# Kernel tuning notes

Hardware: AMD Instinct MI355X
Metric: run time of the kernel (lower is better)

The kernel has to match this reference:

```python
import jax, jax.numpy as jnp
import numpy as np

N, E, F_IN, F_E = 50000, 800000, 128, 16
R, H, C = 4, 4, 32            # num_relations, heads, out_channels
HC = H * C                     # 128
NEG_SLOPE = 0.2                # PyG RGATConv default negative_slope
EPS = 1e-16                    # PyG softmax epsilon


def rgat_conv(x, src, dst, edge_type, edge_attr, w, q, k, e, le, b, concat):
    """Faithful PyG RGATConv (additive-self-attention, across-relation, dim=1, aggr=add).
    x: [N,F]; w: [R,F,H*C]; q,k,e: [H*C,H]; le: [F_e,H*C]; b: bias."""
    n = x.shape[0]
    xw = jnp.einsum('nf,rfo->rno', x, w)              # [R,N,H*C] per-relation projections
    x_i = xw[edge_type, dst]                          # [E,H*C] target-node proj per edge
    x_j = xw[edge_type, src]                          # [E,H*C] source-node proj per edge
    qi = x_i @ q                                      # [E,H]
    kj = x_j @ k + (edge_attr @ le) @ e               # [E,H] (edge features folded into keys)
    alpha = jax.nn.leaky_relu(qi + kj, NEG_SLOPE)     # [E,H]
    # softmax over incoming edges of each destination node (across relations)
    amax = jax.ops.segment_max(alpha, dst, num_segments=n)
    ex = jnp.exp(alpha - amax[dst])
    denom = jax.ops.segment_sum(ex, dst, num_segments=n)
    alpha = ex / (denom[dst] + EPS)
    msg = alpha[:, :, None] * x_j.reshape(-1, H, C)   # [E,H,C]
    out = jax.ops.segment_sum(msg, dst, num_segments=n)  # [N,H,C] sum aggregation
    out = out.reshape(n, H * C) if concat else out.mean(axis=1)
    return out + b


def setup_inputs() -> dict:
    key = jax.random.key(0)
    ks = jax.random.split(key, 18)
    p = 0.05
    inp = {
        'x': jax.random.normal(ks[0], (N, F_IN), dtype=jnp.float32),
        'edge_index': jax.random.randint(ks[1], (2, E), 0, N, dtype=jnp.int64)
            if jax.config.jax_enable_x64 else jax.random.randint(ks[1], (2, E), 0, N).astype(jnp.int32),
        'edge_attr': jax.random.normal(ks[2], (E, F_E), dtype=jnp.float32),
        'edge_type': jax.random.randint(ks[3], (E,), 0, R).astype(jnp.int32),
        # conv1 params (in=F_IN, concat=True -> bias of size H*C)
        'w1': jax.random.normal(ks[4], (R, F_IN, HC), dtype=jnp.float32) * p,
        'q1': jax.random.normal(ks[5], (HC, H), dtype=jnp.float32) * p,
        'k1': jax.random.normal(ks[6], (HC, H), dtype=jnp.float32) * p,
        'e1': jax.random.normal(ks[7], (HC, H), dtype=jnp.float32) * p,
        'le1': jax.random.normal(ks[8], (F_E, HC), dtype=jnp.float32) * p,
        'b1': jnp.zeros((HC,), dtype=jnp.float32),
        # conv3 params (in=H*C=128, concat=False -> bias of size C)
        'w3': jax.random.normal(ks[9], (R, HC, HC), dtype=jnp.float32) * p,
        'q3': jax.random.normal(ks[10], (HC, H), dtype=jnp.float32) * p,
        'k3': jax.random.normal(ks[11], (HC, H), dtype=jnp.float32) * p,
        'e3': jax.random.normal(ks[12], (HC, H), dtype=jnp.float32) * p,
        'le3': jax.random.normal(ks[13], (F_E, HC), dtype=jnp.float32) * p,
        'b3': jnp.zeros((C,), dtype=jnp.float32),
    }
    return inp


def reference(x, edge_index, edge_attr, edge_type,
              w1, q1, k1, e1, le1, b1,
              w3, q3, k3, e3, le3, b3):
    src, dst = edge_index[0], edge_index[1]
    h = jax.nn.relu(rgat_conv(x, src, dst, edge_type, edge_attr,
                              w1, q1, k1, e1, le1, b1, concat=True))
    out = rgat_conv(h, src, dst, edge_type, edge_attr,
                    w3, q3, k3, e3, le3, b3, concat=False)
    return out
```

## Files before the change

kernel.cpp:

```cpp
#include <hip/hip_runtime.h>


#define NEG_SLOPE 0.2f
#define SOFT_EPS 1e-16f

typedef __attribute__((ext_vector_type(8))) short bf16x8;
typedef __attribute__((ext_vector_type(4))) float f32x4;
typedef __attribute__((ext_vector_type(4))) unsigned short u16x4;
typedef __attribute__((ext_vector_type(4))) _Float16 half4;
typedef __attribute__((ext_vector_type(8))) _Float16 half8;

__device__ __forceinline__ void bf16split(float f, unsigned short& h, unsigned short& l) {
  unsigned u = __float_as_uint(f);
  unsigned r = u + 0x7FFFu + ((u >> 16) & 1u);
  h = (unsigned short)(r >> 16);
  float fh = __uint_as_float(((unsigned)h) << 16);
  float d = f - fh;
  unsigned u2 = __float_as_uint(d);
  unsigned r2 = u2 + 0x7FFFu + ((u2 >> 16) & 1u);
  l = (unsigned short)(r2 >> 16);
}


__device__ __forceinline__ void hist_body(int id, const int* __restrict__ dst,
                                          int* __restrict__ deg, int E) {
  int e = id * 256 + (int)threadIdx.x;
  if (e < E) atomicAdd(&deg[dst[e]], 1);
}

__device__ __forceinline__ void convx_body(int id, const float* __restrict__ in,
                                           unsigned short* __restrict__ hi,
                                           unsigned short* __restrict__ lo, int total8) {
  int i = id * 256 + (int)threadIdx.x;
  if (i >= total8) return;
  const float4* p = (const float4*)in + (size_t)i * 2;
  float4 a = p[0], b = p[1];
  float v[8] = {a.x, a.y, a.z, a.w, b.x, b.y, b.z, b.w};
  bf16x8 hv, lv;
#pragma unroll
  for (int j = 0; j < 8; ++j) {
    unsigned short h, l;
    bf16split(v[j], h, l);
    hv[j] = (short)h; lv[j] = (short)l;
  }
  *(bf16x8*)(hi + (size_t)i * 8) = hv;
  *(bf16x8*)(lo + (size_t)i * 8) = lv;
}

__device__ __forceinline__ void convw_body(int idx, const float* __restrict__ w1,
                                           const float* __restrict__ w3,
                                           unsigned short* __restrict__ wF1h,
                                           unsigned short* __restrict__ wF1l,
                                           unsigned short* __restrict__ wF3h,
                                           unsigned short* __restrict__ wF3l) {
  if (idx >= 131072) return;
  int L = idx >> 16;
  int rem = idx & 65535;
  int r = rem >> 14, rem2 = rem & 16383, f = rem2 >> 7, o = rem2 & 127;
  const float* w = L ? w3 : w1;
  unsigned short* dh = L ? wF3h : wF1h;
  unsigned short* dl = L ? wF3l : wF1l;
  float v = w[(r * 128 + f) * 128 + o];
  unsigned short h, l;
  bf16split(v, h, l);
  int ot = o >> 4, c = o & 15, kc = f >> 5, q = (f >> 3) & 3, j = f & 7;
  int di = r * 16384 + ((((ot * 4 + kc) * 4 + q) * 16 + c) * 8 + j);
  dh[di] = h;
  dl[di] = l;
}

__device__ __forceinline__ void wqk_body(int idx, const float* __restrict__ w1,
                                         const float* __restrict__ q1, const float* __restrict__ k1,
                                         const float* __restrict__ w3, const float* __restrict__ q3,
                                         const float* __restrict__ k3, float* __restrict__ wqk) {
  if (idx >= 8192) return;
  int L = idx >> 12, rem = idx & 4095;
  int r = rem >> 10, rem2 = rem & 1023, f = rem2 >> 3, j = rem2 & 7;
  const float* w = L ? w3 : w1;
  const float* qk = (j < 4) ? (L ? q3 : q1) : (L ? k3 : k1);
  int h = j & 3;
  const float* wrow = w + (r * 128 + f) * 128;
  float acc = 0.f;
  for (int o = 0; o < 128; ++o) acc += wrow[o] * qk[o * 4 + h];
  wqk[idx] = acc;
}

__device__ __forceinline__ void lee_body(const float* __restrict__ le1, const float* __restrict__ e1,
                                         const float* __restrict__ le3, const float* __restrict__ e3,
                                         float* __restrict__ lee) {
  int t = threadIdx.x;
  if (t >= 128) return;
  const float* le = (t < 64) ? le1 : le3;
  const float* ee = (t < 64) ? e1 : e3;
  int u = t & 63, f = u >> 2, h = u & 3;
  float acc = 0.f;
  for (int o = 0; o < 128; ++o) acc += le[f * 128 + o] * ee[o * 4 + h];
  lee[t] = acc;
}

__global__ __launch_bounds__(256) void pre_kernel(
    const int* __restrict__ dst, int* __restrict__ deg, int E,
    const float* __restrict__ x, unsigned short* __restrict__ xhi,
    unsigned short* __restrict__ xlo, int total8,
    const float* __restrict__ w1, const float* __restrict__ q1, const float* __restrict__ k1,
    const float* __restrict__ w3, const float* __restrict__ q3, const float* __restrict__ k3,
    float* __restrict__ wqk,
    const float* __restrict__ le1, const float* __restrict__ e1,
    const float* __restrict__ le3, const float* __restrict__ e3, float* __restrict__ lee,
    unsigned short* __restrict__ wF1h, unsigned short* __restrict__ wF1l,
    unsigned short* __restrict__ wF3h, unsigned short* __restrict__ wF3l,
    int nAB, int eb, int cxb) {
  int bid = blockIdx.x;
  if (bid < nAB) {
    int id = bid >> 1;
    if (bid & 1) {
      if (id < eb) hist_body(id, dst, deg, E);
    } else {
      if (id < cxb) convx_body(id, x, xhi, xlo, total8);
    }
  } else {
    int b2 = bid - nAB;
    if (b2 < 512) {
      convw_body(b2 * 256 + (int)threadIdx.x, w1, w3, wF1h, wF1l, wF3h, wF3l);
    } else if (b2 < 544) {
      wqk_body((b2 - 512) * 256 + (int)threadIdx.x, w1, q1, k1, w3, q3, k3, wqk);
    } else {
      lee_body(le1, e1, le3, e3, lee);
    }
  }
}


__global__ __launch_bounds__(256) void scanA_kernel(const int* __restrict__ deg,
                                                    int* __restrict__ bsum, int N) {
  int b = blockIdx.x, t = threadIdx.x;
  int base = b * 1024 + t * 4;
  int s = 0;
#pragma unroll
  for (int j = 0; j < 4; ++j) {
    int i = base + j;
    if (i < N) s += deg[i];
  }
#pragma unroll
  for (int o = 1; o < 64; o <<= 1) s += __shfl_xor(s, o);
  __shared__ int wsum[4];
  if ((t & 63) == 0) wsum[t >> 6] = s;
  __syncthreads();
  if (t == 0) bsum[b] = wsum[0] + wsum[1] + wsum[2] + wsum[3];
}

__global__ __launch_bounds__(256) void scanB_kernel(const int* __restrict__ bsum,
                                                    int* __restrict__ boff,
                                                    int* __restrict__ row_start,
                                                    int nb, int N) {
  int t = threadIdx.x;
  int v = (t < nb) ? bsum[t] : 0;
  int inc = v;
#pragma unroll
  for (int o = 1; o < 64; o <<= 1) {
    int u = __shfl_up(inc, o);
    if ((t & 63) >= o) inc += u;
  }
  __shared__ int wt[4];
  if ((t & 63) == 63) wt[t >> 6] = inc;
  __syncthreads();
  int add = 0;
  for (int wv = 0; wv < (t >> 6); ++wv) add += wt[wv];
  inc += add;
  if (t < nb) boff[t] = inc - v;
  if (t == 255) row_start[N] = inc;
}

__global__ __launch_bounds__(256) void scanC_kernel(const int* __restrict__ deg,
                                                    const int* __restrict__ boff,
                                                    int* __restrict__ row_start,
                                                    int* __restrict__ cursor, int N) {
  int b = blockIdx.x, t = threadIdx.x;
  int base = b * 1024 + t * 4;
  int d[4];
  int s = 0;
#pragma unroll
  for (int j = 0; j < 4; ++j) {
    int i = base + j;
    d[j] = (i < N) ? deg[i] : 0;
    s += d[j];
  }
  int inc = s;
#pragma unroll
  for (int o = 1; o < 64; o <<= 1) {
    int u = __shfl_up(inc, o);
    if ((t & 63) >= o) inc += u;
  }
  __shared__ int wt[4];
  if ((t & 63) == 63) wt[t >> 6] = inc;
  __syncthreads();
  int add = boff[b];
  for (int wv = 0; wv < (t >> 6); ++wv) add += wt[wv];
  int off = add + inc - s;
#pragma unroll
  for (int j = 0; j < 4; ++j) {
    int i = base + j;
    if (i < N) {
      row_start[i] = off;
      cursor[i] = off;
      off += d[j];
    }
  }
}


__device__ __forceinline__ void scatter_body(int id, const int* __restrict__ src,
                                             const int* __restrict__ dst,
                                             const int* __restrict__ et,
                                             int* __restrict__ cursor,
                                             int4* __restrict__ es, int E) {
  int e = id * 256 + (int)threadIdx.x;
  if (e >= E) return;
  int d = dst[e];
  int pos = atomicAdd(&cursor[d], 1);
  es[pos] = make_int4(src[e], d, et[e], e);
}

__device__ __forceinline__ void qkx_body(int nbid, char* smem, const float* __restrict__ xin,
                                         const float* __restrict__ wqk, float* __restrict__ qn,
                                         float* __restrict__ kn, int N) {
  float* swqk = (float*)smem;
  int t = threadIdx.x;
#pragma unroll
  for (int j = 0; j < 16; ++j) {
    int i = j * 256 + t;
    swqk[(i >> 10) * 1032 + (i & 1023)] = wqk[i];
  }
  __syncthreads();
  int nb = nbid * 64;
  int rl = t >> 2, r = t & 3;
  int n = nb + rl;
  int nc = n < N ? n : N - 1;
  const float4* xr = (const float4*)(xin + (size_t)nc * 128);
  const float* wb = swqk + r * 1032;
  float aq0 = 0, aq1 = 0, aq2 = 0, aq3 = 0;
  float ak0 = 0, ak1 = 0, ak2 = 0, ak3 = 0;
#pragma unroll 4
  for (int f4 = 0; f4 < 32; ++f4) {
    float4 xv = xr[f4];
    const float* w0 = wb + f4 * 32;
    float4 qa = *(const float4*)(w0);
    float4 ka = *(const float4*)(w0 + 4);
    float4 qb = *(const float4*)(w0 + 8);
    float4 kb = *(const float4*)(w0 + 12);
    float4 qc = *(const float4*)(w0 + 16);
    float4 kc = *(const float4*)(w0 + 20);
    float4 qd = *(const float4*)(w0 + 24);
    float4 kd = *(const float4*)(w0 + 28);
    aq0 += xv.x * qa.x + xv.y * qb.x + xv.z * qc.x + xv.w * qd.x;
    aq1 += xv.x * qa.y + xv.y * qb.y + xv.z * qc.y + xv.w * qd.y;
    aq2 += xv.x * qa.z + xv.y * qb.z + xv.z * qc.z + xv.w * qd.z;
    aq3 += xv.x * qa.w + xv.y * qb.w + xv.z * qc.w + xv.w * qd.w;
    ak0 += xv.x * ka.x + xv.y * kb.x + xv.z * kc.x + xv.w * kd.x;
    ak1 += xv.x * ka.y + xv.y * kb.y + xv.z * kc.y + xv.w * kd.y;
    ak2 += xv.x * ka.z + xv.y * kb.z + xv.z * kc.z + xv.w * kd.z;
    ak3 += xv.x * ka.w + xv.y * kb.w + xv.z * kc.w + xv.w * kd.w;
  }
  if (n < N) {
    *(float4*)(qn + ((size_t)r * N + n) * 4) = make_float4(aq0, aq1, aq2, aq3);
    *(float4*)(kn + ((size_t)r * N + n) * 4) = make_float4(ak0, ak1, ak2, ak3);
  }
}

__global__ __launch_bounds__(256) void sc_kernel(
    const int* __restrict__ src, const int* __restrict__ dst, const int* __restrict__ et,
    int* __restrict__ cursor, int4* __restrict__ es, int E,
    const float* __restrict__ xin, const float* __restrict__ wqk,
    float* __restrict__ qn, float* __restrict__ kn, int N, int qxb) {
  extern __shared__ char smem[];
  int bid = blockIdx.x;
  int g = bid / 5, r5 = bid - g * 5;
  if (r5 == 4) {
    if (g < qxb) qkx_body(g, smem, xin, wqk, qn, kn, N);
  } else {
    scatter_body(g * 4 + r5, src, dst, et, cursor, es, E);
  }
}


__device__ __forceinline__ void ek2_body(int id, char* smem, const int4* __restrict__ es,
                                         const float* __restrict__ ea,
                                         const float* __restrict__ lee,
                                         float* __restrict__ eks1, float* __restrict__ eks3,
                                         int E) {
  float* sl = (float*)smem;
  if (threadIdx.x < 128) sl[threadIdx.x] = lee[threadIdx.x];
  __syncthreads();
  int i = id * 256 + (int)threadIdx.x;
  if (i >= E) return;
  int eid = es[i].w;
  const float4* a4 = (const float4*)(ea + (size_t)eid * 16);
  float a1[4] = {0, 0, 0, 0}, a3[4] = {0, 0, 0, 0};
#pragma unroll
  for (int ii = 0; ii < 4; ++ii) {
    float4 v = a4[ii];
    int f = ii * 4;
#pragma unroll
    for (int h = 0; h < 4; ++h) {
      a1[h] += v.x * sl[f * 4 + h] + v.y * sl[(f + 1) * 4 + h] +
               v.z * sl[(f + 2) * 4 + h] + v.w * sl[(f + 3) * 4 + h];
      a3[h] += v.x * sl[64 + f * 4 + h] + v.y * sl[64 + (f + 1) * 4 + h] +
               v.z * sl[64 + (f + 2) * 4 + h] + v.w * sl[64 + (f + 3) * 4 + h];
    }
  }
  *(float4*)(eks1 + (size_t)i * 4) = make_float4(a1[0], a1[1], a1[2], a1[3]);
  *(float4*)(eks3 + (size_t)i * 4) = make_float4(a3[0], a3[1], a3[2], a3[3]);
}

__device__ __forceinline__ void proj_body(int pid, char* smem,
                                          const unsigned short* __restrict__ xhi,
                                          const unsigned short* __restrict__ xlo,
                                          const unsigned short* __restrict__ wFh,
                                          const unsigned short* __restrict__ wFl,
                                          _Float16* __restrict__ xwh, int N) {
  bf16x8* wl_h = (bf16x8*)smem;
  bf16x8* wl_l = wl_h + 1024;
  int r = pid & 3;
  int h0 = (pid >> 2) & 1;
  int nb = (pid >> 3) * 128;
  int t = threadIdx.x;
  const bf16x8* srcH = (const bf16x8*)(wFh + r * 16384) + h0 * 1024;
  const bf16x8* srcL = (const bf16x8*)(wFl + r * 16384) + h0 * 1024;
#pragma unroll
  for (int j = 0; j < 4; ++j) {
    int i = j * 256 + t;
    wl_h[i] = srcH[i];
    wl_l[i] = srcL[i];
  }
  __syncthreads();

  int wv = t >> 6;
  int lane = t & 63;
  int c = lane & 15, q = lane >> 4;
  int nodebase = nb + wv * 32;
  int n0 = nodebase + c;
  int n1 = nodebase + 16 + c;
  int n0c = n0 < N ? n0 : N - 1;
  int n1c = n1 < N ? n1 : N - 1;

  f32x4 acc[4][2];
#pragma unroll
  for (int ot = 0; ot < 4; ++ot)
#pragma unroll
    for (int nt = 0; nt < 2; ++nt) acc[ot][nt] = (f32x4){0.f, 0.f, 0.f, 0.f};

  bf16x8 xb[2][4];
  {
    int k0 = q * 8;
    xb[0][0] = *(const bf16x8*)(xhi + (size_t)n0c * 128 + k0);
    xb[0][1] = *(const bf16x8*)(xlo + (size_t)n0c * 128 + k0);
    xb[0][2] = *(const bf16x8*)(xhi + (size_t)n1c * 128 + k0);
    xb[0][3] = *(const bf16x8*)(xlo + (size_t)n1c * 128 + k0);
  }
#pragma unroll
  for (int kc = 0; kc < 4; ++kc) {
    if (kc < 3) {
      int k0 = (kc + 1) * 32 + q * 8;
      xb[(kc + 1) & 1][0] = *(const bf16x8*)(xhi + (size_t)n0c * 128 + k0);
      xb[(kc + 1) & 1][1] = *(const bf16x8*)(xlo + (size_t)n0c * 128 + k0);
      xb[(kc + 1) & 1][2] = *(const bf16x8*)(xhi + (size_t)n1c * 128 + k0);
      xb[(kc + 1) & 1][3] = *(const bf16x8*)(xlo + (size_t)n1c * 128 + k0);
    }
    bf16x8 b0h = xb[kc & 1][0], b0l = xb[kc & 1][1];
    bf16x8 b1h = xb[kc & 1][2], b1l = xb[kc & 1][3];
#pragma unroll
    for (int ot = 0; ot < 4; ++ot) {
      int fi = ((ot * 4 + kc) * 4 + q) * 16 + c;
      bf16x8 ah = wl_h[fi];
      bf16x8 al = wl_l[fi];
      acc[ot][0] = __builtin_amdgcn_mfma_f32_16x16x32_bf16(ah, b0h, acc[ot][0], 0, 0, 0);
      acc[ot][0] = __builtin_amdgcn_mfma_f32_16x16x32_bf16(ah, b0l, acc[ot][0], 0, 0, 0);
      acc[ot][0] = __builtin_amdgcn_mfma_f32_16x16x32_bf16(al, b0h, acc[ot][0], 0, 0, 0);
      acc[ot][1] = __builtin_amdgcn_mfma_f32_16x16x32_bf16(ah, b1h, acc[ot][1], 0, 0, 0);
      acc[ot][1] = __builtin_amdgcn_mfma_f32_16x16x32_bf16(ah, b1l, acc[ot][1], 0, 0, 0);
      acc[ot][1] = __builtin_amdgcn_mfma_f32_16x16x32_bf16(al, b1h, acc[ot][1], 0, 0, 0);
    }
  }

#pragma unroll
  for (int nt = 0; nt < 2; ++nt) {
    int n = nodebase + nt * 16 + c;
    if (n < N) {
      _Float16* basep = xwh + ((size_t)r * N + n) * 128 + h0 * 64 + q * 4;
#pragma unroll
      for (int ot = 0; ot < 4; ++ot) {
        f32x4 a = acc[ot][nt];
        half4 hv;
        hv[0] = (_Float16)a.x; hv[1] = (_Float16)a.y;
        hv[2] = (_Float16)a.z; hv[3] = (_Float16)a.w;
        *(half4*)(basep + ot * 16) = hv;
      }
    }
  }
}

__global__ __launch_bounds__(256) void ep1_kernel(
    const int4* __restrict__ es, const float* __restrict__ ea, const float* __restrict__ lee,
    float* __restrict__ eks1, float* __restrict__ eks3, int E,
    const unsigned short* __restrict__ xhi, const unsigned short* __restrict__ xlo,
    const unsigned short* __restrict__ wFh, const unsigned short* __restrict__ wFl,
    _Float16* __restrict__ xwh, int N, int eb, int pjb) {
  extern __shared__ char smem[];
  int bid = blockIdx.x;
  int g = bid / 3, r3 = bid - g * 3;
  if (r3 == 0) {
    if (g < eb) ek2_body(g, smem, es, ea, lee, eks1, eks3, E);
  } else {
    int id = g * 2 + (r3 - 1);
    if (id < pjb) proj_body(id, smem, xhi, xlo, wFh, wFl, xwh, N);
  }
}

__global__ __launch_bounds__(256) void p2_kernel(
    const unsigned short* __restrict__ xhi, const unsigned short* __restrict__ xlo,
    const unsigned short* __restrict__ wFh, const unsigned short* __restrict__ wFl,
    _Float16* __restrict__ xwh, int N,
    const float* __restrict__ xin, const float* __restrict__ wqk,
    float* __restrict__ qn, float* __restrict__ kn, int pjb, int qxb) {
  extern __shared__ char smem[];
  int bid = blockIdx.x;
  int g = bid / 5, r5 = bid - g * 5;
  if (r5 == 4) {
    if (g < qxb) qkx_body(g, smem, xin, wqk, qn, kn, N);
  } else {
    int id = g * 4 + r5;
    if (id < pjb) proj_body(id, smem, xhi, xlo, wFh, wFl, xwh, N);
  }
}


__device__ __forceinline__ float4 edge_alpha(const int4* __restrict__ es,
                                             const float* __restrict__ qn,
                                             const float* __restrict__ kn,
                                             const float* __restrict__ eks,
                                             int i, int d, int N) {
  int4 v = es[i];
  float4 kv = *(const float4*)(kn + (v.z * N + v.x) * 4);
  float4 ev = ((const float4*)eks)[i];
  float4 q4 = *(const float4*)(qn + (v.z * N + d) * 4);
  float4 a = make_float4(q4.x + kv.x + ev.x, q4.y + kv.y + ev.y,
                         q4.z + kv.z + ev.z, q4.w + kv.w + ev.w);
  a.x = a.x > 0.f ? a.x : NEG_SLOPE * a.x;
  a.y = a.y > 0.f ? a.y : NEG_SLOPE * a.y;
  a.z = a.z > 0.f ? a.z : NEG_SLOPE * a.z;
  a.w = a.w > 0.f ? a.w : NEG_SLOPE * a.w;
  return a;
}

__device__ __forceinline__ float4 max4(float4 a, float4 b) {
  return make_float4(fmaxf(a.x, b.x), fmaxf(a.y, b.y), fmaxf(a.z, b.z), fmaxf(a.w, b.w));
}

__global__ __launch_bounds__(256) void agg_kernel(
    const int4* __restrict__ es, const int* __restrict__ row_start,
    const float* __restrict__ qn, const float* __restrict__ kn,
    const float* __restrict__ eks, float* __restrict__ alpha_s,
    const _Float16* __restrict__ xwh, const float* __restrict__ bias,
    float* __restrict__ out, unsigned short* __restrict__ xhi,
    unsigned short* __restrict__ xlo, int N, int concat) {
  int d = blockIdx.x * 16 + (threadIdx.x >> 4);
  if (d >= N) return;
  int ql = threadIdx.x & 15;
  int rs = row_start[d], re = row_start[d + 1];
  int deg = re - rs;
  int h = ql >> 2;

  float acc[8];
#pragma unroll
  for (int j = 0; j < 8; ++j) acc[j] = 0.f;
  float rden = 0.f;

  if (deg > 0) {
    float4 m = make_float4(-1e30f, -1e30f, -1e30f, -1e30f);
    float4 ar0 = m, ar1 = m, ar2 = m, ar3 = m;
    bool fast = (deg <= 64);
    bool v0 = ql < deg, v1 = 16 + ql < deg, v2 = 32 + ql < deg, v3 = 48 + ql < deg;
    if (fast) {
      int dm1 = deg - 1;
      int o0 = v0 ? ql : dm1;
      int o1 = v1 ? 16 + ql : dm1;
      int o2 = v2 ? 32 + ql : dm1;
      int o3 = v3 ? 48 + ql : dm1;
      float4 a0 = edge_alpha(es, qn, kn, eks, rs + o0, d, N);
      float4 a1 = edge_alpha(es, qn, kn, eks, rs + o1, d, N);
      float4 a2 = edge_alpha(es, qn, kn, eks, rs + o2, d, N);
      float4 a3 = edge_alpha(es, qn, kn, eks, rs + o3, d, N);
      if (v0) { ar0 = a0; m = max4(m, a0); }
      if (v1) { ar1 = a1; m = max4(m, a1); }
      if (v2) { ar2 = a2; m = max4(m, a2); }
      if (v3) { ar3 = a3; m = max4(m, a3); }
    } else {
      for (int i = rs + ql; i < re; i += 16) {
        float4 a = edge_alpha(es, qn, kn, eks, i, d, N);
        ((float4*)alpha_s)[i] = a;
        m = max4(m, a);
      }
    }
#pragma unroll
    for (int o = 1; o < 16; o <<= 1) {
      m.x = fmaxf(m.x, __shfl_xor(m.x, o));
      m.y = fmaxf(m.y, __shfl_xor(m.y, o));
      m.z = fmaxf(m.z, __shfl_xor(m.z, o));
      m.w = fmaxf(m.w, __shfl_xor(m.w, o));
    }

    float4 s = make_float4(0.f, 0.f, 0.f, 0.f);
    if (fast) {
#define SWEEPB(V, AR, OFF)                                                   \
      if (V) {                                                               \
        float4 e4 = make_float4(__expf(AR.x - m.x), __expf(AR.y - m.y),      \
                                __expf(AR.z - m.z), __expf(AR.w - m.w));     \
        ((float4*)alpha_s)[rs + OFF + ql] = e4;                              \
        s.x += e4.x; s.y += e4.y; s.z += e4.z; s.w += e4.w;                  \
      }
      SWEEPB(v0, ar0, 0)
      SWEEPB(v1, ar1, 16)
      SWEEPB(v2, ar2, 32)
      SWEEPB(v3, ar3, 48)
#undef SWEEPB
    } else {
      for (int i = rs + ql; i < re; i += 16) {
        float4 a = ((const float4*)alpha_s)[i];
        float4 e4 = make_float4(__expf(a.x - m.x), __expf(a.y - m.y),
                                __expf(a.z - m.z), __expf(a.w - m.w));
        ((float4*)alpha_s)[i] = e4;
        s.x += e4.x; s.y += e4.y; s.z += e4.z; s.w += e4.w;
      }
    }
#pragma unroll
    for (int o = 1; o < 16; o <<= 1) {
      s.x += __shfl_xor(s.x, o); s.y += __shfl_xor(s.y, o);
      s.z += __shfl_xor(s.z, o); s.w += __shfl_xor(s.w, o);
    }
    float smh = (h == 0) ? s.x : (h == 1) ? s.y : (h == 2) ? s.z : s.w;
    rden = 1.f / (smh + SOFT_EPS);

    int e = rs;
    for (; e + 4 <= re; e += 4) {
      int4 a0 = es[e];
      int4 a1 = es[e + 1];
      int4 a2 = es[e + 2];
      int4 a3 = es[e + 3];
      float w0 = alpha_s[e * 4 + h];
      float w1 = alpha_s[(e + 1) * 4 + h];
      float w2 = alpha_s[(e + 2) * 4 + h];
      float w3 = alpha_s[(e + 3) * 4 + h];
      half8 x0 = *(const half8*)(xwh + (a0.z * N + a0.x) * 128 + ql * 8);
      half8 x1 = *(const half8*)(xwh + (a1.z * N + a1.x) * 128 + ql * 8);
      half8 x2 = *(const half8*)(xwh + (a2.z * N + a2.x) * 128 + ql * 8);
      half8 x3 = *(const half8*)(xwh + (a3.z * N + a3.x) * 128 + ql * 8);
#pragma unroll
      for (int j = 0; j < 8; ++j) {
        acc[j] = fmaf((float)x0[j], w0, acc[j]);
        acc[j] = fmaf((float)x1[j], w1, acc[j]);
        acc[j] = fmaf((float)x2[j], w2, acc[j]);
        acc[j] = fmaf((float)x3[j], w3, acc[j]);
      }
    }
    for (; e < re; ++e) {
      int4 a0 = es[e];
      float w0 = alpha_s[e * 4 + h];
      half8 x0 = *(const half8*)(xwh + (a0.z * N + a0.x) * 128 + ql * 8);
#pragma unroll
      for (int j = 0; j < 8; ++j) acc[j] = fmaf((float)x0[j], w0, acc[j]);
    }
  }
#pragma unroll
  for (int j = 0; j < 8; ++j) acc[j] *= rden;

  if (concat) {
    float4 b0 = ((const float4*)bias)[ql * 2];
    float4 b1 = ((const float4*)bias)[ql * 2 + 1];
    float v[8] = {acc[0] + b0.x, acc[1] + b0.y, acc[2] + b0.z, acc[3] + b0.w,
                  acc[4] + b1.x, acc[5] + b1.y, acc[6] + b1.z, acc[7] + b1.w};
    u16x4 hv0, lv0, hv1, lv1;
#pragma unroll
    for (int j = 0; j < 8; ++j) {
      v[j] = v[j] > 0.f ? v[j] : 0.f;
      unsigned short hh, ll;
      bf16split(v[j], hh, ll);
      if (j < 4) { hv0[j] = hh; lv0[j] = ll; }
      else { hv1[j - 4] = hh; lv1[j - 4] = ll; }
    }
    float* orow = out + (size_t)d * 128 + ql * 8;
    *(float4*)orow = make_float4(v[0], v[1], v[2], v[3]);
    *(float4*)(orow + 4) = make_float4(v[4], v[5], v[6], v[7]);
    *(u16x4*)(xhi + (size_t)d * 128 + ql * 8) = hv0;
    *(u16x4*)(xhi + (size_t)d * 128 + ql * 8 + 4) = hv1;
    *(u16x4*)(xlo + (size_t)d * 128 + ql * 8) = lv0;
    *(u16x4*)(xlo + (size_t)d * 128 + ql * 8 + 4) = lv1;
  } else {
#pragma unroll
    for (int j = 0; j < 8; ++j) {
      acc[j] += __shfl_xor(acc[j], 4);
      acc[j] += __shfl_xor(acc[j], 8);
    }
    if (ql < 4) {
      float4 b0 = ((const float4*)bias)[ql * 2];
      float4 b1 = ((const float4*)bias)[ql * 2 + 1];
      float* orow = out + (size_t)d * 32 + ql * 8;
      *(float4*)orow = make_float4(0.25f * acc[0] + b0.x, 0.25f * acc[1] + b0.y,
                                   0.25f * acc[2] + b0.z, 0.25f * acc[3] + b0.w);
      *(float4*)(orow + 4) = make_float4(0.25f * acc[4] + b1.x, 0.25f * acc[5] + b1.y,
                                         0.25f * acc[6] + b1.z, 0.25f * acc[7] + b1.w);
    }
  }
}

extern "C" void kernel_launch(void* const* d_in, const int* in_sizes, int n_in,
                              void* d_out, int out_size, void* d_ws, size_t ws_size,
                              hipStream_t stream) {
  const float* x   = (const float*)d_in[0];
  const int*   ei  = (const int*)d_in[1];
  const float* ea  = (const float*)d_in[2];
  const int*   etp = (const int*)d_in[3];
  const float* w1  = (const float*)d_in[4];
  const float* q1  = (const float*)d_in[5];
  const float* k1  = (const float*)d_in[6];
  const float* e1  = (const float*)d_in[7];
  const float* le1 = (const float*)d_in[8];
  const float* b1  = (const float*)d_in[9];
  const float* w3  = (const float*)d_in[10];
  const float* q3  = (const float*)d_in[11];
  const float* k3  = (const float*)d_in[12];
  const float* e3  = (const float*)d_in[13];
  const float* le3 = (const float*)d_in[14];
  const float* b3  = (const float*)d_in[15];
  const int N = in_sizes[0] / 128;
  const int E = in_sizes[3];
  const int* srcp = ei;
  const int* dstp = ei + E;

  float* ws   = (float*)d_ws;
  _Float16* xwh = (_Float16*)ws;
  float* qn   = ws + (size_t)2 * N * 128;
  float* kn   = qn + (size_t)4 * N * 4;
  float* eks1 = kn + (size_t)4 * N * 4;
  float* eks3 = eks1 + (size_t)E * 4;
  float* alph = eks3 + (size_t)E * 4;
  float* hbuf = alph + (size_t)E * 4;
  float* leeb = hbuf + (size_t)N * 128;
  float* wqkb = leeb + 128;
  int* deg      = (int*)(wqkb + 8192);
  int* rowst    = deg + N;
  int* cursor   = rowst + N + 1;
  int* bsum     = cursor + N;
  int* boff     = bsum + 256;
  uintptr_t pe = (uintptr_t)(boff + 256);
  pe = (pe + 15) & ~(uintptr_t)15;
  int4* es      = (int4*)pe;
  uintptr_t pa = (uintptr_t)(es + E);
  pa = (pa + 255) & ~(uintptr_t)255;
  unsigned short* xhi  = (unsigned short*)pa;
  unsigned short* xlo  = xhi + (size_t)N * 128;
  unsigned short* wF1h = xlo + (size_t)N * 128;
  unsigned short* wF1l = wF1h + 4 * 128 * 128;
  unsigned short* wF3h = wF1l + 4 * 128 * 128;
  unsigned short* wF3l = wF3h + 4 * 128 * 128;
  (void)ws_size; (void)n_in; (void)out_size;

  int eb   = (E + 255) / 256;
  int nb16 = (N + 15) / 16;
  int nbs  = (N + 1023) / 1024;
  int pgy  = (N + 127) / 128;
  int pjb  = 8 * pgy;
  int qxb  = (N + 63) / 64;
  int cxb  = (N * 128 / 8 + 255) / 256;

  hipMemsetAsync(deg, 0, (size_t)N * sizeof(int), stream);

  int M = eb > cxb ? eb : cxb;
  int nAB = 2 * M;
  int preg = nAB + 512 + 32 + 1;
  pre_kernel<<<preg, 256, 0, stream>>>(dstp, deg, E, x, xhi, xlo, N * 128 / 8,
                                       w1, q1, k1, w3, q3, k3, wqkb,
                                       le1, e1, le3, e3, leeb,
                                       wF1h, wF1l, wF3h, wF3l, nAB, eb, cxb);
  scanA_kernel<<<nbs, 256, 0, stream>>>(deg, bsum, N);
  scanB_kernel<<<1, 256, 0, stream>>>(bsum, boff, rowst, nbs, N);
  scanC_kernel<<<nbs, 256, 0, stream>>>(deg, boff, rowst, cursor, N);

  int scq = (eb + 3) / 4;
  int scg = 5 * (scq > qxb ? scq : qxb);
  sc_kernel<<<scg, 256, 16512, stream>>>(srcp, dstp, etp, cursor, es, E,
                                         x, wqkb, qn, kn, N, qxb);

  int pjh = (pjb + 1) / 2;
  int e1grp = eb > pjh ? eb : pjh;
  ep1_kernel<<<3 * e1grp, 256, 32768, stream>>>(es, ea, leeb, eks1, eks3, E,
                                                xhi, xlo, wF1h, wF1l, xwh, N, eb, pjb);

  agg_kernel<<<nb16, 256, 0, stream>>>(es, rowst, qn, kn, eks1, alph, xwh,
                                       b1, hbuf, xhi, xlo, N, 1);

  int pjq = (pjb + 3) / 4;
  int p2grp = pjq > qxb ? pjq : qxb;
  p2_kernel<<<5 * p2grp, 256, 32768, stream>>>(xhi, xlo, wF3h, wF3l, xwh, N,
                                               hbuf, wqkb + 4096, qn, kn, pjb, qxb);

  agg_kernel<<<nb16, 256, 0, stream>>>(es, rowst, qn, kn, eks3, alph, xwh,
                                       b3, (float*)d_out, xhi, xlo, N, 0);
}
```

Measured before the change: 443.2 us.

## Co-schedule layer-1 projection with edge scatter; split edge-key kernel out

The layer-1 node projection (proj_body) no longer shares a launch with the edge-key computation. It now runs in the same launch as the CSR scatter and the q/k node precompute, interleaved 4:1:4 by block index. The edge-key computation becomes its own small kernel that runs after the scatter, since it reads the sorted edge list. The intent is to overlap the compute-heavy projection with the memory-bound scatter. The cost is that every block of the merged launch reserves 32KB of shared memory, which may lower occupancy for the scatter blocks.

```diff
diff --git a/kernel.cpp b/kernel.cpp
--- a/kernel.cpp
+++ b/kernel.cpp
@@ -267,51 +267,6 @@
   }
 }
 
-__global__ __launch_bounds__(256) void sc_kernel(
-    const int* __restrict__ src, const int* __restrict__ dst, const int* __restrict__ et,
-    int* __restrict__ cursor, int4* __restrict__ es, int E,
-    const float* __restrict__ xin, const float* __restrict__ wqk,
-    float* __restrict__ qn, float* __restrict__ kn, int N, int qxb) {
-  extern __shared__ char smem[];
-  int bid = blockIdx.x;
-  int g = bid / 5, r5 = bid - g * 5;
-  if (r5 == 4) {
-    if (g < qxb) qkx_body(g, smem, xin, wqk, qn, kn, N);
-  } else {
-    scatter_body(g * 4 + r5, src, dst, et, cursor, es, E);
-  }
-}
-
-
-__device__ __forceinline__ void ek2_body(int id, char* smem, const int4* __restrict__ es,
-                                         const float* __restrict__ ea,
-                                         const float* __restrict__ lee,
-                                         float* __restrict__ eks1, float* __restrict__ eks3,
-                                         int E) {
-  float* sl = (float*)smem;
-  if (threadIdx.x < 128) sl[threadIdx.x] = lee[threadIdx.x];
-  __syncthreads();
-  int i = id * 256 + (int)threadIdx.x;
-  if (i >= E) return;
-  int eid = es[i].w;
-  const float4* a4 = (const float4*)(ea + (size_t)eid * 16);
-  float a1[4] = {0, 0, 0, 0}, a3[4] = {0, 0, 0, 0};
-#pragma unroll
-  for (int ii = 0; ii < 4; ++ii) {
-    float4 v = a4[ii];
-    int f = ii * 4;
-#pragma unroll
-    for (int h = 0; h < 4; ++h) {
-      a1[h] += v.x * sl[f * 4 + h] + v.y * sl[(f + 1) * 4 + h] +
-               v.z * sl[(f + 2) * 4 + h] + v.w * sl[(f + 3) * 4 + h];
-      a3[h] += v.x * sl[64 + f * 4 + h] + v.y * sl[64 + (f + 1) * 4 + h] +
-               v.z * sl[64 + (f + 2) * 4 + h] + v.w * sl[64 + (f + 3) * 4 + h];
-    }
-  }
-  *(float4*)(eks1 + (size_t)i * 4) = make_float4(a1[0], a1[1], a1[2], a1[3]);
-  *(float4*)(eks3 + (size_t)i * 4) = make_float4(a3[0], a3[1], a3[2], a3[3]);
-}
-
 __device__ __forceinline__ void proj_body(int pid, char* smem,
                                           const unsigned short* __restrict__ xhi,
                                           const unsigned short* __restrict__ xlo,
@@ -399,21 +354,54 @@
   }
 }
 
-__global__ __launch_bounds__(256) void ep1_kernel(
-    const int4* __restrict__ es, const float* __restrict__ ea, const float* __restrict__ lee,
-    float* __restrict__ eks1, float* __restrict__ eks3, int E,
+__global__ __launch_bounds__(256) void sc9_kernel(
+    const int* __restrict__ src, const int* __restrict__ dst, const int* __restrict__ et,
+    int* __restrict__ cursor, int4* __restrict__ es, int E,
+    const float* __restrict__ xin, const float* __restrict__ wqk,
+    float* __restrict__ qn, float* __restrict__ kn, int N, int qxb,
     const unsigned short* __restrict__ xhi, const unsigned short* __restrict__ xlo,
     const unsigned short* __restrict__ wFh, const unsigned short* __restrict__ wFl,
-    _Float16* __restrict__ xwh, int N, int eb, int pjb) {
+    _Float16* __restrict__ xwh, int pjb) {
   extern __shared__ char smem[];
   int bid = blockIdx.x;
-  int g = bid / 3, r3 = bid - g * 3;
-  if (r3 == 0) {
-    if (g < eb) ek2_body(g, smem, es, ea, lee, eks1, eks3, E);
+  int g = bid / 9, r9 = bid - g * 9;
+  if (r9 < 4) {
+    scatter_body(g * 4 + r9, src, dst, et, cursor, es, E);
+  } else if (r9 == 4) {
+    if (g < qxb) qkx_body(g, smem, xin, wqk, qn, kn, N);
   } else {
-    int id = g * 2 + (r3 - 1);
+    int id = g * 4 + (r9 - 5);
     if (id < pjb) proj_body(id, smem, xhi, xlo, wFh, wFl, xwh, N);
   }
+}
+
+
+__global__ __launch_bounds__(256) void ek2_kernel(
+    const int4* __restrict__ es, const float* __restrict__ ea,
+    const float* __restrict__ lee, float* __restrict__ eks1,
+    float* __restrict__ eks3, int E) {
+  __shared__ float sl[128];
+  if (threadIdx.x < 128) sl[threadIdx.x] = lee[threadIdx.x];
+  __syncthreads();
+  int i = blockIdx.x * 256 + (int)threadIdx.x;
+  if (i >= E) return;
+  int eid = es[i].w;
+  const float4* a4 = (const float4*)(ea + (size_t)eid * 16);
+  float a1[4] = {0, 0, 0, 0}, a3[4] = {0, 0, 0, 0};
+#pragma unroll
+  for (int ii = 0; ii < 4; ++ii) {
+    float4 v = a4[ii];
+    int f = ii * 4;
+#pragma unroll
+    for (int h = 0; h < 4; ++h) {
+      a1[h] += v.x * sl[f * 4 + h] + v.y * sl[(f + 1) * 4 + h] +
+               v.z * sl[(f + 2) * 4 + h] + v.w * sl[(f + 3) * 4 + h];
+      a3[h] += v.x * sl[64 + f * 4 + h] + v.y * sl[64 + (f + 1) * 4 + h] +
+               v.z * sl[64 + (f + 2) * 4 + h] + v.w * sl[64 + (f + 3) * 4 + h];
+    }
+  }
+  *(float4*)(eks1 + (size_t)i * 4) = make_float4(a1[0], a1[1], a1[2], a1[3]);
+  *(float4*)(eks3 + (size_t)i * 4) = make_float4(a3[0], a3[1], a3[2], a3[3]);
 }
 
 __global__ __launch_bounds__(256) void p2_kernel(
@@ -686,19 +674,19 @@
   scanC_kernel<<<nbs, 256, 0, stream>>>(deg, boff, rowst, cursor, N);
 
   int scq = (eb + 3) / 4;
-  int scg = 5 * (scq > qxb ? scq : qxb);
-  sc_kernel<<<scg, 256, 16512, stream>>>(srcp, dstp, etp, cursor, es, E,
-                                         x, wqkb, qn, kn, N, qxb);
-
-  int pjh = (pjb + 1) / 2;
-  int e1grp = eb > pjh ? eb : pjh;
-  ep1_kernel<<<3 * e1grp, 256, 32768, stream>>>(es, ea, leeb, eks1, eks3, E,
-                                                xhi, xlo, wF1h, wF1l, xwh, N, eb, pjb);
+  int pjq = (pjb + 3) / 4;
+  int g9 = scq;
+  if (qxb > g9) g9 = qxb;
+  if (pjq > g9) g9 = pjq;
+  sc9_kernel<<<9 * g9, 256, 32768, stream>>>(srcp, dstp, etp, cursor, es, E,
+                                             x, wqkb, qn, kn, N, qxb,
+                                             xhi, xlo, wF1h, wF1l, xwh, pjb);
+
+  ek2_kernel<<<eb, 256, 0, stream>>>(es, ea, leeb, eks1, eks3, E);
 
   agg_kernel<<<nb16, 256, 0, stream>>>(es, rowst, qn, kn, eks1, alph, xwh,
                                        b1, hbuf, xhi, xlo, N, 1);
 
-  int pjq = (pjb + 3) / 4;
   int p2grp = pjq > qxb ? pjq : qxb;
   p2_kernel<<<5 * p2grp, 256, 32768, stream>>>(xhi, xlo, wF3h, wF3l, xwh, N,
                                                hbuf, wqkb + 4096, qn, kn, pjb, qxb);
```

Result: faster. 432.2 us (-2.5%).
